# Kernel tuning notes

Hardware: AMD Instinct MI355X
Metric: run time of the kernel (lower is better)

The kernel has to match this reference:

```python
import jax, jax.numpy as jnp
import numpy as np
from jax import lax

C = 256      # in_c == out_c == dim
NH = 8       # num_heads
K = 7        # depthwise pos-enc kernel
H1 = 512     # int(mlp_ratio * in_c) = 2.0 * 256
B, Hs, Ws = 2, 48, 48


def setup_inputs() -> dict:
    key = jax.random.key(0)
    ks = jax.random.split(key, 8)
    w = lambda k, shape: jax.random.normal(k, shape, jnp.float32) * 0.02
    return {
        "x": jax.random.normal(ks[0], (B, C, Hs, Ws), jnp.float32),
        # 1x1 convs stored as [out, in] (BN folded into weight+bias)
        "qk_w": w(ks[1], (2 * C, C)), "qk_b": jnp.zeros((2 * C,), jnp.float32),
        "v_w": w(ks[2], (C, C)),       "v_b": jnp.zeros((C,), jnp.float32),
        # depthwise positional encoding conv [C,1,K,K]
        "pe_w": w(ks[3], (C, 1, K, K)), "pe_b": jnp.zeros((C,), jnp.float32),
        "proj_w": w(ks[4], (C, C)),    "proj_b": jnp.zeros((C,), jnp.float32),
        # conv FFN: 1x1 (SiLU) -> 1x1 (no act)
        "fc1_w": w(ks[5], (H1, C)),    "fc1_b": jnp.zeros((H1,), jnp.float32),
        "fc2_w": w(ks[6], (C, H1)),    "fc2_b": jnp.zeros((C,), jnp.float32),
    }


def _c1(x, w, b):
    # 1x1 conv == per-pixel matmul
    return jnp.einsum('bchw,oc->bohw', x, w) + b[None, :, None, None]


def reference(x, qk_w, qk_b, v_w, v_b, pe_w, pe_b, proj_w, proj_b,
              fc1_w, fc1_b, fc2_w, fc2_b):
    Bb, Cc, Hh, Ww = x.shape
    hd = Cc // NH                 # head_dim = 32
    N = Hh * Ww
    scale = hd ** -0.5

    # ---- AttentionV2 ----
    qk = _c1(x, qk_w, qk_b).reshape(Bb, NH, 2 * hd, N)
    q, k = qk[:, :, :hd], qk[:, :, hd:]
    v_full = _c1(x, v_w, v_b)                      # [B,C,H,W]
    pe = lax.conv_general_dilated(
        v_full, pe_w, (1, 1), 'SAME', feature_group_count=Cc,
        dimension_numbers=('NCHW', 'OIHW', 'NCHW')) + pe_b[None, :, None, None]
    v = v_full.reshape(Bb, NH, hd, N)

    # attn = q^T @ k * scale ; softmax over keys
    attn = jax.nn.softmax(jnp.einsum('bhdn,bhdm->bhnm', q, k) * scale, axis=-1)
    o = jnp.einsum('bhdm,bhnm->bhdn', v, attn).reshape(Bb, Cc, Hh, Ww)
    attn_out = _c1(o + pe, proj_w, proj_b)

    # ---- block residuals + conv FFN (add=True) ----
    x1 = x + attn_out
    h = jax.nn.silu(_c1(x1, fc1_w, fc1_b))         # Conv(in_c, hidden, 1, 1) with SiLU
    return x1 + _c1(h, fc2_w, fc2_b)               # Conv(hidden, out_c, 1, act=False)
```

## Files before the change

kernel.cpp:

```cpp
#include <hip/hip_runtime.h>
#include <hip/hip_bf16.h>

#define NCH 256
#define NHD 8
#define HD 32
#define NPIX 2304
#define H1DIM 512

typedef __attribute__((ext_vector_type(8))) __bf16 bf16x8;
typedef __attribute__((ext_vector_type(4))) float f32x4;

__global__ __launch_bounds__(256) void prep_k(
    const float* __restrict__ x,
    const float* __restrict__ w0, const float* __restrict__ w1,
    const float* __restrict__ w2, const float* __restrict__ w3,
    const float* __restrict__ w4,
    __bf16* __restrict__ Xb, __bf16* __restrict__ Wall) {
    const int tid = threadIdx.x;
    if (blockIdx.x < 288) {
        const int t = blockIdx.x;
        const int b = t / 144, r0 = t % 144;
        const int c0 = (r0 / 36) * 64, n0 = (r0 % 36) * 64;
        __shared__ float tile[64][65];
        const size_t sb = ((size_t)b * NCH + c0) * NPIX + n0;
#pragma unroll
        for (int i = 0; i < 16; ++i) {
            int idx = tid + i * 256;
            int rr = idx >> 6, cc = idx & 63;
            tile[rr][cc] = x[sb + (size_t)rr * NPIX + cc];
        }
        __syncthreads();
#pragma unroll
        for (int i = 0; i < 8; ++i) {
            int idx = tid + i * 256;
            int nn = idx >> 5, cp = (idx & 31) * 2;
            union { __bf16 h[2]; unsigned u; } pk;
            pk.h[0] = (__bf16)tile[cp][nn];
            pk.h[1] = (__bf16)tile[cp + 1][nn];
            *(unsigned*)&Xb[((size_t)b * NPIX + n0 + nn) * NCH + c0 + cp] = pk.u;
        }
    } else {
        int i = (blockIdx.x - 288) * 256 + tid;
        const float* src; int off;
        if (i < 32768)      { src = w0; off = i; }
        else if (i < 49152) { src = w1; off = i - 32768; }
        else if (i < 65536) { src = w2; off = i - 49152; }
        else if (i < 98304) { src = w3; off = i - 65536; }
        else                { src = w4; off = i - 98304; }
        float4 v = ((const float4*)src)[off];
        union { __bf16 h[4]; uint2 u; } pk;
        pk.h[0] = (__bf16)v.x; pk.h[1] = (__bf16)v.y;
        pk.h[2] = (__bf16)v.z; pk.h[3] = (__bf16)v.w;
        ((uint2*)Wall)[i] = pk.u;
    }
}

__global__ __launch_bounds__(256) void qkv_k(
    const __bf16* __restrict__ A, const __bf16* __restrict__ Wq,
    const __bf16* __restrict__ Wv, const float* __restrict__ qk_b,
    const float* __restrict__ v_b, __bf16* __restrict__ Qb,
    __bf16* __restrict__ Kf, float* __restrict__ v_bu,
    __bf16* __restrict__ Vf) {
    const int tid = threadIdx.x;
    const int wave = tid >> 6, lane = tid & 63;
    const int l16 = lane & 15, quad = lane >> 4;
    const int m0 = blockIdx.x * 32;
    const int idx = blockIdx.y * 4 + wave;
    const int b = blockIdx.z;
    const bool isv = idx >= 32;
    const int oc0 = (isv ? idx - 32 : idx) * 16;
    const __bf16* W = isv ? Wv : Wq;

    const __bf16* aptr = A + ((size_t)b * NPIX + m0 + l16) * NCH + quad * 8;
    const __bf16* bptr = W + (size_t)(oc0 + l16) * NCH + quad * 8;

    f32x4 acc0 = {0.f,0.f,0.f,0.f}, acc1 = {0.f,0.f,0.f,0.f};
#pragma unroll 8
    for (int k = 0; k < NCH; k += 32) {
        bf16x8 bf = *(const bf16x8*)(bptr + k);
        bf16x8 a0 = *(const bf16x8*)(aptr + k);
        bf16x8 a1 = *(const bf16x8*)(aptr + (size_t)16 * NCH + k);
        acc0 = __builtin_amdgcn_mfma_f32_16x16x32_bf16(a0, bf, acc0, 0, 0, 0);
        acc1 = __builtin_amdgcn_mfma_f32_16x16x32_bf16(a1, bf, acc1, 0, 0, 0);
    }

    const int oc = oc0 + l16;
#pragma unroll
    for (int mh = 0; mh < 2; ++mh) {
        const f32x4 acc = mh ? acc1 : acc0;
        const int m0h = m0 + mh * 16;
        const int mb = m0h + quad * 4;
        const int px16 = m0h >> 4;
        if (!isv) {
            const float bb = qk_b[oc];
            const int bh = b * NHD + (oc0 >> 6);
            const int dd = (oc0 & 16) + l16;
            if ((oc0 & 32) == 0) {
                const float qs = 0.17677669529663689f * 1.4426950408889634f;
#pragma unroll
                for (int r = 0; r < 4; ++r)
                    Qb[((size_t)bh * NPIX + mb + r) * 32 + dd] = (__bf16)((acc[r] + bb) * qs);
            } else {
                __bf16* kp = Kf + ((size_t)(bh * 144 + px16) * 64 + (dd >> 3) * 16 + quad * 4) * 8 + (dd & 7);
#pragma unroll
                for (int r = 0; r < 4; ++r) kp[r * 8] = (__bf16)(acc[r] + bb);
            }
        } else {
            const float bb = v_b[oc];
            const int bh = b * NHD + (oc0 >> 5);
            const int half = (oc0 >> 4) & 1;
            const size_t fb = ((size_t)b * NCH + oc) * NPIX + mb;
            float4 vf_; float* vp = &vf_.x;
            union { __bf16 hh[4]; uint2 u; } pk;
#pragma unroll
            for (int r = 0; r < 4; ++r) {
                float v = acc[r] + bb;
                vp[r] = v; pk.hh[r] = (__bf16)v;
            }
            *(float4*)&v_bu[fb] = vf_;
            *(uint2*)&Vf[((size_t)(bh * 144 + px16) * 64 + lane) * 8 + half * 4] = pk.u;
        }
    }
}

template <int IC, int OC, int MODE>
__global__ __launch_bounds__(256) void convmm_k(
    const __bf16* __restrict__ A, const __bf16* __restrict__ W,
    const float* __restrict__ bias, const float* __restrict__ resid,
    float* __restrict__ out_f, __bf16* __restrict__ out_b) {
    const int tid = threadIdx.x;
    const int wave = tid >> 6, lane = tid & 63;
    const int l16 = lane & 15, quad = lane >> 4;
    const int m0 = blockIdx.x * 32;
    const int oc0 = (blockIdx.y * 4 + wave) * 16;
    const int b = blockIdx.z;

    const __bf16* aptr = A + ((size_t)b * NPIX + m0 + l16) * IC + quad * 8;
    const __bf16* bptr = W + (size_t)(oc0 + l16) * IC + quad * 8;

    f32x4 acc0 = {0.f,0.f,0.f,0.f}, acc1 = {0.f,0.f,0.f,0.f};
#pragma unroll 8
    for (int k = 0; k < IC; k += 32) {
        bf16x8 bf = *(const bf16x8*)(bptr + k);
        bf16x8 a0 = *(const bf16x8*)(aptr + k);
        bf16x8 a1 = *(const bf16x8*)(aptr + (size_t)16 * IC + k);
        acc0 = __builtin_amdgcn_mfma_f32_16x16x32_bf16(a0, bf, acc0, 0, 0, 0);
        acc1 = __builtin_amdgcn_mfma_f32_16x16x32_bf16(a1, bf, acc1, 0, 0, 0);
    }

    const int oc = oc0 + l16;
    const float bb = bias[oc];
#pragma unroll
    for (int mh = 0; mh < 2; ++mh) {
        const f32x4 acc = mh ? acc1 : acc0;
        const int mb = m0 + mh * 16 + quad * 4;
        if constexpr (MODE == 2) {
            const size_t fb = ((size_t)b * OC + oc) * NPIX + mb;
            float4 xr = *(const float4*)&resid[fb];
            const float* xp = &xr.x;
            float4 vf_; float* vp = &vf_.x;
#pragma unroll
            for (int r = 0; r < 4; ++r) {
                float v = acc[r] + bb + xp[r];
                vp[r] = v;
                out_b[((size_t)b * NPIX + mb + r) * OC + oc] = (__bf16)v;
            }
            *(float4*)&out_f[fb] = vf_;
        } else if constexpr (MODE == 3) {
#pragma unroll
            for (int r = 0; r < 4; ++r) {
                float v = acc[r] + bb;
                v = v / (1.f + __expf(-v));
                out_b[((size_t)b * NPIX + mb + r) * OC + oc] = (__bf16)v;
            }
        } else {
            const size_t fb = ((size_t)b * OC + oc) * NPIX + mb;
            float4 xr = *(const float4*)&resid[fb];
            const float* xp = &xr.x;
            float4 vf_; float* vp = &vf_.x;
#pragma unroll
            for (int r = 0; r < 4; ++r) vp[r] = acc[r] + bb + xp[r];
            *(float4*)&out_f[fb] = vf_;
        }
    }
}

__global__ __launch_bounds__(256) void dwconv_k(const float* __restrict__ vb,
                                                const float* __restrict__ pw,
                                                const float* __restrict__ pb,
                                                float* __restrict__ pe) {
    const int c = blockIdx.x, b = blockIdx.y, tid = threadIdx.x;
    __shared__ float plane[NPIX];
    __shared__ float wk[49];
    const size_t base = ((size_t)b * NCH + c) * NPIX;
    for (int i = tid; i < NPIX; i += 256) plane[i] = vb[base + i];
    if (tid < 49) wk[tid] = pw[c * 49 + tid];
    float bb = pb[c];
    __syncthreads();
    for (int p = tid; p < NPIX; p += 256) {
        int y = p / 48, x = p - y * 48;
        float s = bb;
#pragma unroll
        for (int ky = 0; ky < 7; ++ky) {
            int yy = y + ky - 3;
            if ((unsigned)yy < 48u) {
#pragma unroll
                for (int kx = 0; kx < 7; ++kx) {
                    int xx = x + kx - 3;
                    if ((unsigned)xx < 48u) s += wk[ky * 7 + kx] * plane[yy * 48 + xx];
                }
            }
        }
        pe[base + p] = s;
    }
}

__global__ __launch_bounds__(512, 4) void attn7_k(const __bf16* __restrict__ Qb,
                                                  const __bf16* __restrict__ Kf,
                                                  const __bf16* __restrict__ Vf,
                                                  const float* __restrict__ pe,
                                                  __bf16* __restrict__ opb) {
    const int tid = threadIdx.x;
    const int wave = tid >> 6, lane = tid & 63;
    const int l16 = lane & 15, quad = lane >> 4;
    const int qb = blockIdx.x * 64;
    const int h = blockIdx.y, b = blockIdx.z;
    const int bh = b * NHD + h;

    __shared__ float o_s[8][32][65];
    __shared__ float l_s[8][64];

    bf16x8 b_q[4];
#pragma unroll
    for (int g = 0; g < 4; ++g)
        b_q[g] = *(const bf16x8*)(Qb + ((size_t)bh * NPIX + qb + g * 16 + l16) * 32 + quad * 8);

    const __bf16* kf = Kf + ((size_t)(bh * 144 + wave * 18) * 64 + lane) * 8;
    const __bf16* vf = Vf + ((size_t)(bh * 144 + wave * 18) * 64 + lane) * 8;

    f32x4 oacc[4][2];
    f32x4 lacc[4];
#pragma unroll
    for (int g = 0; g < 4; ++g) {
        oacc[g][0] = {0.f,0.f,0.f,0.f};
        oacc[g][1] = {0.f,0.f,0.f,0.f};
        lacc[g] = {0.f,0.f,0.f,0.f};
    }

#pragma unroll 2
    for (int t = 0; t < 18; ++t) {
        bf16x8 a_k = *(const bf16x8*)(kf + (size_t)t * 512);
        bf16x8 va  = *(const bf16x8*)(vf + (size_t)t * 512);
#pragma unroll
        for (int g = 0; g < 4; ++g) {
            f32x4 z = {0.f, 0.f, 0.f, 0.f};
            f32x4 s = __builtin_amdgcn_mfma_f32_16x16x32_bf16(a_k, b_q[g], z, 0, 0, 0);
            f32x4 p;
#pragma unroll
            for (int r = 0; r < 4; ++r) p[r] = __builtin_amdgcn_exp2f(s[r]);
            lacc[g] += p;
            bf16x8 blo = {}, bhi = {};
#pragma unroll
            for (int r = 0; r < 4; ++r) {
                __bf16 c = (__bf16)p[r];
                blo[r] = c; bhi[4 + r] = c;
            }
            oacc[g][0] = __builtin_amdgcn_mfma_f32_16x16x32_bf16(va, blo, oacc[g][0], 0, 0, 0);
            oacc[g][1] = __builtin_amdgcn_mfma_f32_16x16x32_bf16(va, bhi, oacc[g][1], 0, 0, 0);
        }
    }

#pragma unroll
    for (int g = 0; g < 4; ++g) {
        float ls = lacc[g][0] + lacc[g][1] + lacc[g][2] + lacc[g][3];
        ls += __shfl_xor(ls, 16); ls += __shfl_xor(ls, 32);
        if (quad == 0) l_s[wave][g * 16 + l16] = ls;
#pragma unroll
        for (int half = 0; half < 2; ++half)
#pragma unroll
            for (int r = 0; r < 4; ++r)
                o_s[wave][half * 16 + quad * 4 + r][g * 16 + l16] = oacc[g][half][r];
    }
    __syncthreads();

    const int q = lane;
    const int d0 = wave * 4;
    float l = 0.f;
#pragma unroll
    for (int w = 0; w < 8; ++w) l += l_s[w][q];
    const float inv = 1.f / l;
    const int n = qb + q;
    union { __bf16 hh[4]; uint2 u; } pk;
#pragma unroll
    for (int j = 0; j < 4; ++j) {
        float v = 0.f;
#pragma unroll
        for (int w = 0; w < 8; ++w) v += o_s[w][d0 + j][q];
        v = v * inv + pe[((size_t)b * NCH + h * HD + d0 + j) * NPIX + n];
        pk.hh[j] = (__bf16)v;
    }
    *(uint2*)&opb[((size_t)b * NPIX + n) * NCH + h * HD + d0] = pk.u;
}

extern "C" void kernel_launch(void* const* d_in, const int* in_sizes, int n_in,
                              void* d_out, int out_size, void* d_ws, size_t ws_size,
                              hipStream_t stream) {
    const float* x    = (const float*)d_in[0];
    const float* qk_w = (const float*)d_in[1];
    const float* qk_b = (const float*)d_in[2];
    const float* v_w  = (const float*)d_in[3];
    const float* v_b  = (const float*)d_in[4];
    const float* pe_w = (const float*)d_in[5];
    const float* pe_b = (const float*)d_in[6];
    const float* pj_w = (const float*)d_in[7];
    const float* pj_b = (const float*)d_in[8];
    const float* f1_w = (const float*)d_in[9];
    const float* f1_b = (const float*)d_in[10];
    const float* f2_w = (const float*)d_in[11];
    const float* f2_b = (const float*)d_in[12];
    float* out = (float*)d_out;

    const int B = 2;
    const size_t plane = (size_t)NCH * NPIX;
    const size_t bp = (size_t)B * plane;

    float* v_bu  = (float*)d_ws;
    float* pe_bu = v_bu + bp;
    float* x1_f  = pe_bu + bp;
    __bf16* Xb   = (__bf16*)(x1_f + bp);
    __bf16* opb  = Xb + bp;
    __bf16* x1b  = opb + bp;
    __bf16* hb   = x1b + bp;
    __bf16* Qb   = hb + 2 * bp;
    __bf16* Kf   = Qb + bp;
    __bf16* Vf   = Kf + bp;
    __bf16* Wall = Vf + bp;
    __bf16* Wq = Wall;
    __bf16* Wv = Wall + 131072;
    __bf16* Wp = Wall + 196608;
    __bf16* W1 = Wall + 262144;
    __bf16* W2 = Wall + 393216;

    prep_k<<<800, 256, 0, stream>>>(x, qk_w, v_w, pj_w, f1_w, f2_w, Xb, Wall);
    qkv_k<<<dim3(72, 12, B), 256, 0, stream>>>(Xb, Wq, Wv, qk_b, v_b, Qb, Kf, v_bu, Vf);
    dwconv_k<<<dim3(NCH, B), 256, 0, stream>>>(v_bu, pe_w, pe_b, pe_bu);
    attn7_k<<<dim3(36, NHD, B), 512, 0, stream>>>(Qb, Kf, Vf, pe_bu, opb);
    convmm_k<256, 256, 2><<<dim3(72, 4, B), 256, 0, stream>>>(opb, Wp, pj_b, x, x1_f, x1b);
    convmm_k<256, 512, 3><<<dim3(72, 8, B), 256, 0, stream>>>(x1b, W1, f1_b, nullptr, nullptr, hb);
    convmm_k<512, 256, 4><<<dim3(72, 4, B), 256, 0, stream>>>(hb, W2, f2_b, x1_f, out, nullptr);
}
```

Before: 210.0 us.

## Pack two key tiles per PV MFMA and prefetch K/V fragments

```diff
diff --git a/kernel.cpp b/kernel.cpp
--- a/kernel.cpp
+++ b/kernel.cpp
@@ -118,7 +118,8 @@
                 vp[r] = v; pk.hh[r] = (__bf16)v;
             }
             *(float4*)&v_bu[fb] = vf_;
-            *(uint2*)&Vf[((size_t)(bh * 144 + px16) * 64 + lane) * 8 + half * 4] = pk.u;
+            const int G = px16 >> 1, sub = px16 & 1;
+            *(uint2*)&Vf[(((size_t)(bh * 72 + G) * 2 + half) * 64 + lane) * 8 + sub * 4] = pk.u;
         }
     }
 }
@@ -215,7 +216,7 @@
     }
 }
 
-__global__ __launch_bounds__(512, 4) void attn7_k(const __bf16* __restrict__ Qb,
+__global__ __launch_bounds__(512, 4) void attn8_k(const __bf16* __restrict__ Qb,
                                                   const __bf16* __restrict__ Kf,
                                                   const __bf16* __restrict__ Vf,
                                                   const float* __restrict__ pe,
@@ -227,7 +228,7 @@
     const int h = blockIdx.y, b = blockIdx.z;
     const int bh = b * NHD + h;
 
-    __shared__ float o_s[8][32][65];
+    __shared__ float o_s[8][32][66];
     __shared__ float l_s[8][64];
 
     bf16x8 b_q[4];
@@ -236,7 +237,7 @@
         b_q[g] = *(const bf16x8*)(Qb + ((size_t)bh * NPIX + qb + g * 16 + l16) * 32 + quad * 8);
 
     const __bf16* kf = Kf + ((size_t)(bh * 144 + wave * 18) * 64 + lane) * 8;
-    const __bf16* vf = Vf + ((size_t)(bh * 144 + wave * 18) * 64 + lane) * 8;
+    const __bf16* vf = Vf + (((size_t)(bh * 72 + wave * 9) * 2) * 64 + lane) * 8;
 
     f32x4 oacc[4][2];
     f32x4 lacc[4];
@@ -247,27 +248,42 @@
         lacc[g] = {0.f,0.f,0.f,0.f};
     }
 
-#pragma unroll 2
-    for (int t = 0; t < 18; ++t) {
-        bf16x8 a_k = *(const bf16x8*)(kf + (size_t)t * 512);
-        bf16x8 va  = *(const bf16x8*)(vf + (size_t)t * 512);
+    bf16x8 k0 = *(const bf16x8*)(kf);
+    bf16x8 k1 = *(const bf16x8*)(kf + 512);
+    bf16x8 v0 = *(const bf16x8*)(vf);
+    bf16x8 v1 = *(const bf16x8*)(vf + 512);
+
+    for (int t = 0; t < 9; ++t) {
+        bf16x8 nk0, nk1, nv0, nv1;
+        if (t < 8) {
+            const size_t o = (size_t)(t + 1) * 1024;
+            nk0 = *(const bf16x8*)(kf + o);
+            nk1 = *(const bf16x8*)(kf + o + 512);
+            nv0 = *(const bf16x8*)(vf + o);
+            nv1 = *(const bf16x8*)(vf + o + 512);
+        }
 #pragma unroll
         for (int g = 0; g < 4; ++g) {
             f32x4 z = {0.f, 0.f, 0.f, 0.f};
-            f32x4 s = __builtin_amdgcn_mfma_f32_16x16x32_bf16(a_k, b_q[g], z, 0, 0, 0);
-            f32x4 p;
-#pragma unroll
-            for (int r = 0; r < 4; ++r) p[r] = __builtin_amdgcn_exp2f(s[r]);
-            lacc[g] += p;
-            bf16x8 blo = {}, bhi = {};
-#pragma unroll
-            for (int r = 0; r < 4; ++r) {
-                __bf16 c = (__bf16)p[r];
-                blo[r] = c; bhi[4 + r] = c;
-            }
-            oacc[g][0] = __builtin_amdgcn_mfma_f32_16x16x32_bf16(va, blo, oacc[g][0], 0, 0, 0);
-            oacc[g][1] = __builtin_amdgcn_mfma_f32_16x16x32_bf16(va, bhi, oacc[g][1], 0, 0, 0);
-        }
+            f32x4 s0 = __builtin_amdgcn_mfma_f32_16x16x32_bf16(k0, b_q[g], z, 0, 0, 0);
+            f32x4 s1 = __builtin_amdgcn_mfma_f32_16x16x32_bf16(k1, b_q[g], z, 0, 0, 0);
+            f32x4 p0, p1;
+#pragma unroll
+            for (int r = 0; r < 4; ++r) {
+                p0[r] = __builtin_amdgcn_exp2f(s0[r]);
+                p1[r] = __builtin_amdgcn_exp2f(s1[r]);
+            }
+            lacc[g] += p0 + p1;
+            bf16x8 bfrag;
+#pragma unroll
+            for (int r = 0; r < 4; ++r) {
+                bfrag[r]     = (__bf16)p0[r];
+                bfrag[4 + r] = (__bf16)p1[r];
+            }
+            oacc[g][0] = __builtin_amdgcn_mfma_f32_16x16x32_bf16(v0, bfrag, oacc[g][0], 0, 0, 0);
+            oacc[g][1] = __builtin_amdgcn_mfma_f32_16x16x32_bf16(v1, bfrag, oacc[g][1], 0, 0, 0);
+        }
+        k0 = nk0; k1 = nk1; v0 = nv0; v1 = nv1;
     }
 
 #pragma unroll
@@ -344,7 +360,7 @@
     prep_k<<<800, 256, 0, stream>>>(x, qk_w, v_w, pj_w, f1_w, f2_w, Xb, Wall);
     qkv_k<<<dim3(72, 12, B), 256, 0, stream>>>(Xb, Wq, Wv, qk_b, v_b, Qb, Kf, v_bu, Vf);
     dwconv_k<<<dim3(NCH, B), 256, 0, stream>>>(v_bu, pe_w, pe_b, pe_bu);
-    attn7_k<<<dim3(36, NHD, B), 512, 0, stream>>>(Qb, Kf, Vf, pe_bu, opb);
+    attn8_k<<<dim3(36, NHD, B), 512, 0, stream>>>(Qb, Kf, Vf, pe_bu, opb);
     convmm_k<256, 256, 2><<<dim3(72, 4, B), 256, 0, stream>>>(opb, Wp, pj_b, x, x1_f, x1b);
     convmm_k<256, 512, 3><<<dim3(72, 8, B), 256, 0, stream>>>(x1b, W1, f1_b, nullptr, nullptr, hb);
     convmm_k<512, 256, 4><<<dim3(72, 4, B), 256, 0, stream>>>(hb, W2, f2_b, x1_f, out, nullptr);
```

Result: slower. 257.6 us (+22.7%).
